# Optimization experiments

Hardware: AMD Instinct MI355X
Metric: run time of the kernel (lower is better)

## Reference

```python
import jax, jax.numpy as jnp
import numpy as np


def setup_inputs() -> dict:
    key = jax.random.key(0)
    k1, k2, k3, k4 = jax.random.split(key, 4)
    N, Ck, Cv, T, H, W = 8, 128, 512, 8, 30, 30
    return {
        "q_key": jax.random.normal(k1, (N, Ck, H, W), dtype=jnp.float32),
        "q_val": jax.random.normal(k2, (N, Cv, H, W), dtype=jnp.float32),
        "m_key": jax.random.normal(k3, (N, Ck, T, H, W), dtype=jnp.float32),
        "m_val": jax.random.normal(k4, (N, Cv, T, H, W), dtype=jnp.float32),
    }


def reference(q_key, q_val, m_key, m_val):
    N, Ck, H, W = q_key.shape
    _, Cv, T, Hm, Wm = m_val.shape
    qk = q_key.reshape(N, Ck, H * W)            # n c q
    mk = m_key.reshape(N, Ck, T * Hm * Wm)      # n c m
    # affinity [n, q, m], scaled by 1/sqrt(Ck)
    aff = jnp.einsum("ncq,ncm->nqm", qk, mk) * (Ck ** -0.5)
    # NOTE: softmax over the QUERY axis (axis=1), per the original module
    attn = jax.nn.softmax(aff, axis=1)
    mv = m_val.reshape(N, Cv, T * Hm * Wm)      # n c m
    mapped = jnp.einsum("nqm,ncm->ncq", attn, mv).reshape(N, Cv, Hm, Wm)
    return jnp.concatenate([q_val, mapped], axis=1)  # [N, 2*Cv, H, W]
```

## Files before the change

kernel.cpp:

```cpp
#include <hip/hip_runtime.h>
#include <stdint.h>

#define N_  8
#define CK  128
#define CV  512
#define HW  900
#define M_  7200
#define QK_SCALE 0.08838834764831845f

typedef __attribute__((ext_vector_type(8))) short  short8;
typedef __attribute__((ext_vector_type(4))) float  floatx4;
typedef __attribute__((ext_vector_type(4))) unsigned int   uintx4;
typedef __attribute__((ext_vector_type(4))) unsigned short ushortx4;

__device__ __forceinline__ uint16_t f32_to_bf16(float x) {
    union { float f; uint32_t u; } v; v.f = x;
    return (uint16_t)((v.u + 0x7FFFu + ((v.u >> 16) & 1u)) >> 16);
}

__device__ __forceinline__ void gload_lds16(const uint16_t* g, short* l) {
    __builtin_amdgcn_global_load_lds(
        (const __attribute__((address_space(1))) void*)g,
        (__attribute__((address_space(3))) void*)l,
        16, 0, 0);
}

__global__ void k_zero(float* __restrict__ p) {
    int i = blockIdx.x * 256 + threadIdx.x;
    if (i < N_ * M_) p[i] = 0.f;
}

__global__ __launch_bounds__(256) void k_copy_qval(const float* __restrict__ qv,
                                                   float* __restrict__ out) {
    unsigned i = blockIdx.x * 256 + threadIdx.x;
    unsigned e = i * 4u;
    unsigned n = e / (CV * HW);
    unsigned off = e - n * (CV * HW);
    *(floatx4*)&out[(size_t)n * (2 * CV * HW) + off] = *(const floatx4*)&qv[e];
}

__global__ __launch_bounds__(256) void k_trans(const float* __restrict__ in,
                                               uint16_t* __restrict__ outp, int L) {
    __shared__ float tile[32][33];
    const int tx = threadIdx.x & 31;
    const int ty = threadIdx.x >> 5;
    const int l0 = blockIdx.x * 32;
    const int c0 = blockIdx.y * 32;
    const int n  = blockIdx.z;
    const float* src = in + (size_t)n * CK * L;
    uint16_t* dst = outp + (size_t)n * L * CK;
#pragma unroll
    for (int p = 0; p < 4; p++) {
        int c = c0 + p * 8 + ty;
        int l = l0 + tx;
        float v = 0.f;
        if (l < L) v = src[(size_t)c * L + l];
        tile[p * 8 + ty][tx] = v;
    }
    __syncthreads();
#pragma unroll
    for (int p = 0; p < 4; p++) {
        int l = l0 + p * 8 + ty;
        int c = c0 + tx;
        if (l < L) dst[(size_t)l * CK + c] = f32_to_bf16(tile[tx][p * 8 + ty]);
    }
}

#define K1_TS 144

__global__ __launch_bounds__(256) void k1_gemm_exp(
    const uint16_t* __restrict__ qkT,
    const uint16_t* __restrict__ mkT,
    uint16_t* __restrict__ E,
    float* __restrict__ dsum)
{
    __shared__ __align__(16) short smem[18432];
    __shared__ float colsum[128];
    short* ldsA = smem;
    short* ldsB = smem + 8192;

    const int m0 = blockIdx.x * 128;
    const int q0 = blockIdx.y * 128;
    const int n  = blockIdx.z;
    const int tid = threadIdx.x;

    if (tid < 128) colsum[tid] = 0.f;

    const int lane = tid & 63;
    const int wid  = tid >> 6;
    const int wq   = (wid >> 1) << 6;
    const int wm   = (wid & 1) << 6;
    const int fr   = lane & 15;
    const int quad = lane >> 4;

    int sr[4], sc[4];
#pragma unroll
    for (int j = 0; j < 4; j++) {
        int s = ((wid * 4 + j) << 9) + lane * 8;
        sr[j] = s >> 6;
        sc[j] = s & 63;
    }

    floatx4 acc[4][4];
#pragma unroll
    for (int a = 0; a < 4; a++)
#pragma unroll
        for (int b = 0; b < 4; b++) acc[a][b] = (floatx4){0.f, 0.f, 0.f, 0.f};

    const uint16_t* Ab = qkT + (size_t)n * HW * CK;
    const uint16_t* Bb = mkT + (size_t)n * M_ * CK;

#pragma unroll
    for (int kc = 0; kc < 2; kc++) {
        __syncthreads();
#pragma unroll
        for (int j = 0; j < 4; j++)
            gload_lds16(&Ab[(size_t)(q0 + sr[j]) * CK + kc * 64 + sc[j]],
                        ldsA + (wid * 4 + j) * 512);
#pragma unroll
        for (int j = 0; j < 4; j++)
            gload_lds16(&Bb[(size_t)(m0 + sr[j]) * CK + kc * 64 + sc[j]],
                        ldsB + (wid * 4 + j) * 512);
        __syncthreads();
#pragma unroll
        for (int ks = 0; ks < 2; ks++) {
            const int k0 = ks * 32 + quad * 8;
            short8 af[4], bfr[4];
#pragma unroll
            for (int t = 0; t < 4; t++)
                af[t] = *(const short8*)&ldsA[(wq + t * 16 + fr) * 64 + k0];
#pragma unroll
            for (int t = 0; t < 4; t++)
                bfr[t] = *(const short8*)&ldsB[(wm + t * 16 + fr) * 64 + k0];
#pragma unroll
            for (int tq = 0; tq < 4; tq++)
#pragma unroll
                for (int tm = 0; tm < 4; tm++)
                    acc[tq][tm] = __builtin_amdgcn_mfma_f32_16x16x32_bf16(
                        af[tq], bfr[tm], acc[tq][tm], 0, 0, 0);
        }
    }

    __syncthreads();
    float cs[4] = {0.f, 0.f, 0.f, 0.f};
#pragma unroll
    for (int tq = 0; tq < 4; tq++) {
#pragma unroll
        for (int tm = 0; tm < 4; tm++) {
            const int col = wm + tm * 16 + fr;
#pragma unroll
            for (int i = 0; i < 4; i++) {
                const int row = wq + tq * 16 + quad * 4 + i;
                float e = __expf(acc[tq][tm][i] * QK_SCALE);
                if (q0 + row < HW) cs[tm] += e;
                smem[row * K1_TS + col] = (short)f32_to_bf16(e);
            }
        }
    }
#pragma unroll
    for (int tm = 0; tm < 4; tm++) {
        float s = cs[tm];
        s += __shfl_xor(s, 16, 64);
        s += __shfl_xor(s, 32, 64);
        if (quad == 0) atomicAdd(&colsum[wm + tm * 16 + fr], s);
    }
    __syncthreads();

    uint16_t* En = E + (size_t)n * HW * M_;
#pragma unroll
    for (int j = 0; j < 8; j++) {
        int idx = tid + j * 256;
        int r   = idx >> 4;
        int c8  = (idx & 15) * 8;
        if (q0 + r < HW && m0 + c8 + 8 <= M_) {
            uintx4 v = *(const uintx4*)&smem[r * K1_TS + c8];
            *(uintx4*)&En[(size_t)(q0 + r) * M_ + m0 + c8] = v;
        }
    }
    if (tid < 128) {
        const int gm = m0 + tid;
        if (gm < M_) atomicAdd(&dsum[(size_t)n * M_ + gm], colsum[tid]);
    }
}

__global__ void k_dinv(const float* __restrict__ d, float* __restrict__ di) {
    int i = blockIdx.x * 256 + threadIdx.x;
    if (i < N_ * M_) di[i] = 1.0f / d[i];
}

__global__ __launch_bounds__(256) void k_mvs(
    const float* __restrict__ mval,
    const float* __restrict__ dinv,
    uint16_t* __restrict__ mvs)
{
    unsigned i = blockIdx.x * 256 + threadIdx.x;
    unsigned base = i * 4u;
    unsigned n = base / (unsigned)(CV * M_);
    unsigned m = base % (unsigned)M_;
    floatx4 v  = *(const floatx4*)&mval[base];
    floatx4 di = *(const floatx4*)&dinv[n * (unsigned)M_ + m];
    ushortx4 o;
    o[0] = f32_to_bf16(v[0] * di[0]);
    o[1] = f32_to_bf16(v[1] * di[1]);
    o[2] = f32_to_bf16(v[2] * di[2]);
    o[3] = f32_to_bf16(v[3] * di[3]);
    *(ushortx4*)&mvs[base] = o;
}

#define K2_SPLITS 3
#define K2_STEPS 25

__global__ __launch_bounds__(256) void k2_split3(
    const uint16_t* __restrict__ mvs,
    const uint16_t* __restrict__ E,
    float* __restrict__ partials)
{
    __shared__ __align__(16) short ldsA[128 * 96];
    __shared__ __align__(16) short ldsB[128 * 96];

    const int q0 = blockIdx.x * 128;
    const int c0 = blockIdx.y * 128;
    const int nz = blockIdx.z;
    const int n     = nz / K2_SPLITS;
    const int split = nz - n * K2_SPLITS;
    const int tid = threadIdx.x;

    const int lane = tid & 63;
    const int wid  = tid >> 6;
    const int wc   = (wid >> 1) << 6;
    const int wq   = (wid & 1) << 6;
    const int fr   = lane & 15;
    const int quad = lane >> 4;

    int sr[6], sc[6];
#pragma unroll
    for (int j = 0; j < 6; j++) {
        int s = ((wid * 6 + j) << 9) + lane * 8;
        sr[j] = s / 96;
        sc[j] = s - sr[j] * 96;
    }

    floatx4 acc[4][4];
#pragma unroll
    for (int a = 0; a < 4; a++)
#pragma unroll
        for (int b = 0; b < 4; b++) acc[a][b] = (floatx4){0.f, 0.f, 0.f, 0.f};

    const uint16_t* Asrc = mvs + (size_t)(n * CV + c0) * M_ + split * 2400;
    const uint16_t* Bsrc = E + (size_t)n * HW * M_ + split * 2400;

    for (int step = 0; step < K2_STEPS; step++) {
        const int m0 = step * 96;
        __syncthreads();
#pragma unroll
        for (int j = 0; j < 6; j++)
            gload_lds16(&Asrc[(size_t)sr[j] * M_ + m0 + sc[j]],
                        ldsA + (wid * 6 + j) * 512);
#pragma unroll
        for (int j = 0; j < 6; j++)
            gload_lds16(&Bsrc[(size_t)(q0 + sr[j]) * M_ + m0 + sc[j]],
                        ldsB + (wid * 6 + j) * 512);
        __syncthreads();
#pragma unroll
        for (int ks = 0; ks < 3; ks++) {
            const int k0 = ks * 32 + quad * 8;
            short8 af[4], bfr[4];
#pragma unroll
            for (int t = 0; t < 4; t++)
                af[t] = *(const short8*)&ldsA[(wc + t * 16 + fr) * 96 + k0];
#pragma unroll
            for (int t = 0; t < 4; t++)
                bfr[t] = *(const short8*)&ldsB[(wq + t * 16 + fr) * 96 + k0];
#pragma unroll
            for (int tc = 0; tc < 4; tc++)
#pragma unroll
                for (int tq = 0; tq < 4; tq++)
                    acc[tc][tq] = __builtin_amdgcn_mfma_f32_16x16x32_bf16(
                        af[tc], bfr[tq], acc[tc][tq], 0, 0, 0);
        }
    }

    float* P = partials + ((size_t)split * N_ + n) * CV * HW;
#pragma unroll
    for (int tc = 0; tc < 4; tc++) {
#pragma unroll
        for (int tq = 0; tq < 4; tq++) {
            const int gq = q0 + wq + tq * 16 + fr;
            if (gq < HW) {
#pragma unroll
                for (int i = 0; i < 4; i++) {
                    const int gc = c0 + wc + tc * 16 + quad * 4 + i;
                    P[(size_t)gc * HW + gq] = acc[tc][tq][i];
                }
            }
        }
    }
}

__global__ __launch_bounds__(256) void k_reduce3(const float* __restrict__ partials,
                                                 float* __restrict__ out) {
    unsigned i = blockIdx.x * 256 + threadIdx.x;
    unsigned e = i * 4u;
    unsigned n = e / (CV * HW);
    unsigned off = e - n * (CV * HW);
    const size_t stride = (size_t)N_ * CV * HW;
    const float* p = partials + (size_t)n * CV * HW + off;
    floatx4 a = *(const floatx4*)&p[0];
    floatx4 b = *(const floatx4*)&p[stride];
    floatx4 c = *(const floatx4*)&p[2 * stride];
    floatx4 s = a + b + c;
    *(floatx4*)&out[(size_t)n * (2 * CV * HW) + CV * HW + off] = s;
}

extern "C" void kernel_launch(void* const* d_in, const int* in_sizes, int n_in,
                              void* d_out, int out_size, void* d_ws, size_t ws_size,
                              hipStream_t stream) {
    const float* qkey = (const float*)d_in[0];
    const float* qval = (const float*)d_in[1];
    const float* mkey = (const float*)d_in[2];
    const float* mval = (const float*)d_in[3];
    float* out = (float*)d_out;

    char* ws = (char*)d_ws;
    uint16_t* E        = (uint16_t*)ws;
    float*    dsum     = (float*)(ws + 103680000);
    float*    dinv     = (float*)(ws + 103910400);
    uint16_t* mvs      = (uint16_t*)(ws + 104140800);
    float*    partials = (float*)(ws + 163123200);
    uint16_t* qkT      = (uint16_t*)(ws + 163123200);
    uint16_t* mkT      = (uint16_t*)(ws + 163123200 + 1843200);

    (void)in_sizes; (void)n_in; (void)out_size; (void)ws_size;

    k_zero<<<dim3((N_ * M_ + 255) / 256), 256, 0, stream>>>(dsum);
    k_copy_qval<<<dim3((N_ * CV * HW) / 4 / 256), 256, 0, stream>>>(qval, out);
    k_trans<<<dim3(29, 4, N_), 256, 0, stream>>>(qkey, qkT, HW);
    k_trans<<<dim3(225, 4, N_), 256, 0, stream>>>(mkey, mkT, M_);
    k1_gemm_exp<<<dim3(57, 8, N_), 256, 0, stream>>>(qkT, mkT, E, dsum);
    k_dinv<<<dim3((N_ * M_ + 255) / 256), 256, 0, stream>>>(dsum, dinv);
    k_mvs<<<dim3((N_ * CV * M_) / 4 / 256), 256, 0, stream>>>(mval, dinv, mvs);
    k2_split3<<<dim3(8, 4, N_ * K2_SPLITS), 256, 0, stream>>>(mvs, E, partials);
    k_reduce3<<<dim3((N_ * CV * HW) / 4 / 256), 256, 0, stream>>>(partials, out);
}
```

Measured before the change: 414.1 us.

## Double-buffer LDS loads in both GEMM kernels and swizzle block order

Both MFMA GEMM kernels switch from single-buffered 64/96-wide K tiles, which used two barriers per step, to double-buffered 32-wide K tiles. The next tile's global-to-LDS loads are issued before the current tile is computed, so load latency can overlap with MFMA work and one barrier per step is removed. The block index is also remapped with a swizzle so that concurrently scheduled blocks share input rows, which is meant to improve L2 reuse. In exchange the K tiles are narrower and there are more loop iterations, and the swizzle assumes fixed grid dimensions (57x8x8 and 8x4x24).

```diff
diff --git a/kernel.cpp b/kernel.cpp
--- a/kernel.cpp
+++ b/kernel.cpp
@@ -76,12 +76,14 @@
 {
     __shared__ __align__(16) short smem[18432];
     __shared__ float colsum[128];
-    short* ldsA = smem;
-    short* ldsB = smem + 8192;
-
-    const int m0 = blockIdx.x * 128;
-    const int q0 = blockIdx.y * 128;
-    const int n  = blockIdx.z;
+
+    const int bid = blockIdx.x + 57 * (blockIdx.y + 8 * blockIdx.z);
+    const int swz = (bid & 7) * 456 + (bid >> 3);
+    const int mb   = swz % 57;
+    const int rest = swz / 57;
+    const int m0 = mb * 128;
+    const int q0 = (rest & 7) * 128;
+    const int n  = rest >> 3;
     const int tid = threadIdx.x;
 
     if (tid < 128) colsum[tid] = 0.f;
@@ -93,53 +95,53 @@
     const int fr   = lane & 15;
     const int quad = lane >> 4;
 
-    int sr[4], sc[4];
-#pragma unroll
-    for (int j = 0; j < 4; j++) {
-        int s = ((wid * 4 + j) << 9) + lane * 8;
-        sr[j] = s >> 6;
-        sc[j] = s & 63;
-    }
-
-    floatx4 acc[4][4];
-#pragma unroll
-    for (int a = 0; a < 4; a++)
-#pragma unroll
-        for (int b = 0; b < 4; b++) acc[a][b] = (floatx4){0.f, 0.f, 0.f, 0.f};
+    const int ca = wid * 2;
+    const int rr = lane >> 2;
+    const int cc = (lane & 3) * 8;
 
     const uint16_t* Ab = qkT + (size_t)n * HW * CK;
     const uint16_t* Bb = mkT + (size_t)n * M_ * CK;
-
-#pragma unroll
-    for (int kc = 0; kc < 2; kc++) {
-        __syncthreads();
-#pragma unroll
-        for (int j = 0; j < 4; j++)
-            gload_lds16(&Ab[(size_t)(q0 + sr[j]) * CK + kc * 64 + sc[j]],
-                        ldsA + (wid * 4 + j) * 512);
-#pragma unroll
-        for (int j = 0; j < 4; j++)
-            gload_lds16(&Bb[(size_t)(m0 + sr[j]) * CK + kc * 64 + sc[j]],
-                        ldsB + (wid * 4 + j) * 512);
-        __syncthreads();
-#pragma unroll
-        for (int ks = 0; ks < 2; ks++) {
-            const int k0 = ks * 32 + quad * 8;
-            short8 af[4], bfr[4];
-#pragma unroll
-            for (int t = 0; t < 4; t++)
-                af[t] = *(const short8*)&ldsA[(wq + t * 16 + fr) * 64 + k0];
-#pragma unroll
-            for (int t = 0; t < 4; t++)
-                bfr[t] = *(const short8*)&ldsB[(wm + t * 16 + fr) * 64 + k0];
-#pragma unroll
-            for (int tq = 0; tq < 4; tq++)
-#pragma unroll
-                for (int tm = 0; tm < 4; tm++)
-                    acc[tq][tm] = __builtin_amdgcn_mfma_f32_16x16x32_bf16(
-                        af[tq], bfr[tm], acc[tq][tm], 0, 0, 0);
-        }
-    }
+    const uint16_t* A0p = Ab + (size_t)(q0 + ca * 16 + rr) * CK + cc;
+    const uint16_t* A1p = A0p + 16 * CK;
+    const uint16_t* B0p = Bb + (size_t)(m0 + ca * 16 + rr) * CK + cc;
+    const uint16_t* B1p = B0p + 16 * CK;
+
+    floatx4 acc[4][4];
+#pragma unroll
+    for (int a = 0; a < 4; a++)
+#pragma unroll
+        for (int b = 0; b < 4; b++) acc[a][b] = (floatx4){0.f, 0.f, 0.f, 0.f};
+
+#define K1_STAGE(buf, ko) do { \
+    gload_lds16(A0p + (ko), smem + (buf) * 4096 + ca * 512); \
+    gload_lds16(A1p + (ko), smem + (buf) * 4096 + ca * 512 + 512); \
+    gload_lds16(B0p + (ko), smem + 8192 + (buf) * 4096 + ca * 512); \
+    gload_lds16(B1p + (ko), smem + 8192 + (buf) * 4096 + ca * 512 + 512); \
+} while (0)
+
+#define K1_COMPUTE(buf) do { \
+    const int k0 = quad * 8; \
+    short8 af[4], bfr[4]; \
+    _Pragma("unroll") \
+    for (int t = 0; t < 4; t++) \
+        af[t] = *(const short8*)&smem[(buf) * 4096 + (wq + t * 16 + fr) * 32 + k0]; \
+    _Pragma("unroll") \
+    for (int t = 0; t < 4; t++) \
+        bfr[t] = *(const short8*)&smem[8192 + (buf) * 4096 + (wm + t * 16 + fr) * 32 + k0]; \
+    _Pragma("unroll") \
+    for (int tq = 0; tq < 4; tq++) \
+        _Pragma("unroll") \
+        for (int tm = 0; tm < 4; tm++) \
+            acc[tq][tm] = __builtin_amdgcn_mfma_f32_16x16x32_bf16( \
+                af[tq], bfr[tm], acc[tq][tm], 0, 0, 0); \
+} while (0)
+
+    K1_STAGE(0, 0);
+    __syncthreads();
+    K1_STAGE(1, 32); K1_COMPUTE(0); __syncthreads();
+    K1_STAGE(0, 64); K1_COMPUTE(1); __syncthreads();
+    K1_STAGE(1, 96); K1_COMPUTE(0); __syncthreads();
+    K1_COMPUTE(1);
 
     __syncthreads();
     float cs[4] = {0.f, 0.f, 0.f, 0.f};
@@ -181,6 +183,8 @@
         const int gm = m0 + tid;
         if (gm < M_) atomicAdd(&dsum[(size_t)n * M_ + gm], colsum[tid]);
     }
+#undef K1_STAGE
+#undef K1_COMPUTE
 }
 
 __global__ void k_dinv(const float* __restrict__ d, float* __restrict__ di) {
@@ -208,19 +212,21 @@
 }
 
 #define K2_SPLITS 3
-#define K2_STEPS 25
+#define K2_BK 32
+#define K2_STEPS 75
 
 __global__ __launch_bounds__(256) void k2_split3(
     const uint16_t* __restrict__ mvs,
     const uint16_t* __restrict__ E,
     float* __restrict__ partials)
 {
-    __shared__ __align__(16) short ldsA[128 * 96];
-    __shared__ __align__(16) short ldsB[128 * 96];
-
-    const int q0 = blockIdx.x * 128;
-    const int c0 = blockIdx.y * 128;
-    const int nz = blockIdx.z;
+    __shared__ __align__(16) short lds2[16384];
+
+    const int bid = blockIdx.x + 8 * (blockIdx.y + 4 * blockIdx.z);
+    const int swz = (bid & 7) * 96 + (bid >> 3);
+    const int q0 = (swz & 7) << 7;
+    const int c0 = ((swz >> 3) & 3) << 7;
+    const int nz = swz >> 5;
     const int n     = nz / K2_SPLITS;
     const int split = nz - n * K2_SPLITS;
     const int tid = threadIdx.x;
@@ -232,53 +238,58 @@
     const int fr   = lane & 15;
     const int quad = lane >> 4;
 
-    int sr[6], sc[6];
-#pragma unroll
-    for (int j = 0; j < 6; j++) {
-        int s = ((wid * 6 + j) << 9) + lane * 8;
-        sr[j] = s / 96;
-        sc[j] = s - sr[j] * 96;
-    }
-
-    floatx4 acc[4][4];
-#pragma unroll
-    for (int a = 0; a < 4; a++)
-#pragma unroll
-        for (int b = 0; b < 4; b++) acc[a][b] = (floatx4){0.f, 0.f, 0.f, 0.f};
+    const int ca = wid * 2;
+    const int rr = lane >> 2;
+    const int cc = (lane & 3) * 8;
 
     const uint16_t* Asrc = mvs + (size_t)(n * CV + c0) * M_ + split * 2400;
     const uint16_t* Bsrc = E + (size_t)n * HW * M_ + split * 2400;
-
-    for (int step = 0; step < K2_STEPS; step++) {
-        const int m0 = step * 96;
+    const uint16_t* A0p = Asrc + (size_t)(ca * 16 + rr) * M_ + cc;
+    const uint16_t* A1p = A0p + (size_t)16 * M_;
+    const uint16_t* B0p = Bsrc + (size_t)(q0 + ca * 16 + rr) * M_ + cc;
+    const uint16_t* B1p = B0p + (size_t)16 * M_;
+
+    floatx4 acc[4][4];
+#pragma unroll
+    for (int a = 0; a < 4; a++)
+#pragma unroll
+        for (int b = 0; b < 4; b++) acc[a][b] = (floatx4){0.f, 0.f, 0.f, 0.f};
+
+#define K2_STAGE(buf, mo) do { \
+    gload_lds16(A0p + (mo), lds2 + (buf) * 4096 + ca * 512); \
+    gload_lds16(A1p + (mo), lds2 + (buf) * 4096 + ca * 512 + 512); \
+    gload_lds16(B0p + (mo), lds2 + 8192 + (buf) * 4096 + ca * 512); \
+    gload_lds16(B1p + (mo), lds2 + 8192 + (buf) * 4096 + ca * 512 + 512); \
+} while (0)
+
+#define K2_COMPUTE(buf) do { \
+    const int k0 = quad * 8; \
+    short8 af[4], bfr[4]; \
+    _Pragma("unroll") \
+    for (int t = 0; t < 4; t++) \
+        af[t] = *(const short8*)&lds2[(buf) * 4096 + (wc + t * 16 + fr) * 32 + k0]; \
+    _Pragma("unroll") \
+    for (int t = 0; t < 4; t++) \
+        bfr[t] = *(const short8*)&lds2[8192 + (buf) * 4096 + (wq + t * 16 + fr) * 32 + k0]; \
+    _Pragma("unroll") \
+    for (int tc = 0; tc < 4; tc++) \
+        _Pragma("unroll") \
+        for (int tq = 0; tq < 4; tq++) \
+            acc[tc][tq] = __builtin_amdgcn_mfma_f32_16x16x32_bf16( \
+                af[tc], bfr[tq], acc[tc][tq], 0, 0, 0); \
+} while (0)
+
+    K2_STAGE(0, 0);
+    __syncthreads();
+    for (int s = 0; s < K2_STEPS - 1; s += 2) {
+        K2_STAGE(1, (s + 1) * K2_BK);
+        K2_COMPUTE(0);
         __syncthreads();
-#pragma unroll
-        for (int j = 0; j < 6; j++)
-            gload_lds16(&Asrc[(size_t)sr[j] * M_ + m0 + sc[j]],
-                        ldsA + (wid * 6 + j) * 512);
-#pragma unroll
-        for (int j = 0; j < 6; j++)
-            gload_lds16(&Bsrc[(size_t)(q0 + sr[j]) * M_ + m0 + sc[j]],
-                        ldsB + (wid * 6 + j) * 512);
+        K2_STAGE(0, (s + 2) * K2_BK);
+        K2_COMPUTE(1);
         __syncthreads();
-#pragma unroll
-        for (int ks = 0; ks < 3; ks++) {
-            const int k0 = ks * 32 + quad * 8;
-            short8 af[4], bfr[4];
-#pragma unroll
-            for (int t = 0; t < 4; t++)
-                af[t] = *(const short8*)&ldsA[(wc + t * 16 + fr) * 96 + k0];
-#pragma unroll
-            for (int t = 0; t < 4; t++)
-                bfr[t] = *(const short8*)&ldsB[(wq + t * 16 + fr) * 96 + k0];
-#pragma unroll
-            for (int tc = 0; tc < 4; tc++)
-#pragma unroll
-                for (int tq = 0; tq < 4; tq++)
-                    acc[tc][tq] = __builtin_amdgcn_mfma_f32_16x16x32_bf16(
-                        af[tc], bfr[tq], acc[tc][tq], 0, 0, 0);
-        }
-    }
+    }
+    K2_COMPUTE(0);
 
     float* P = partials + ((size_t)split * N_ + n) * CV * HW;
 #pragma unroll
@@ -295,6 +306,8 @@
             }
         }
     }
+#undef K2_STAGE
+#undef K2_COMPUTE
 }
 
 __global__ __launch_bounds__(256) void k_reduce3(const float* __restrict__ partials,
```

New measurement: 419.4 us. Within noise of the previous version (+1.3%).
